# Kernel optimization log

Measured on AMD Instinct MI355X. Metric: run time of the kernel, lower is better.

## Reference

```python
import jax, jax.numpy as jnp
import numpy as np

TEMPERATURE = 0.07
NEG = -1e9  # stand-in for -inf on the diagonal; exp(NEG) == 0


def setup_inputs() -> dict:
    key = jax.random.key(0)
    k1, k2, k3 = jax.random.split(key, 3)
    B, D = 4096, 1024
    return {
        "anchor_features": jax.random.normal(k1, (B, D), dtype=jnp.float32),
        "positive_features": jax.random.normal(k2, (B, D), dtype=jnp.float32),
        "labels": jax.random.randint(k3, (B,), 0, 2),
    }


def reference(anchor_features, positive_features, labels):
    B = anchor_features.shape[0]
    # L2-normalize (normalize=True)
    a = anchor_features / jnp.linalg.norm(anchor_features, axis=1, keepdims=True)
    p = positive_features / jnp.linalg.norm(positive_features, axis=1, keepdims=True)
    feats = jnp.concatenate([a, p], axis=0)                      # [2B, D]
    sim = jnp.matmul(feats, feats.T) / TEMPERATURE               # [2B, 2B]
    diag = jnp.eye(2 * B, dtype=bool)
    sim = jnp.where(diag, NEG, sim)                              # mask self-similarity
    # logsumexp over all non-self entries per row (diag contributes exp(NEG)=0)
    lse = jax.nn.logsumexp(sim, axis=1)                          # [2B]
    # positive pair similarity: sim[i, i+B] == sim[i+B, i] == <a_i, p_i>/t
    cross = jnp.sum(a * p, axis=1) / TEMPERATURE                 # [B]
    pos_sim = jnp.concatenate([cross, cross])                    # [2B]
    lab = jnp.concatenate([labels, labels]).astype(sim.dtype)    # [2B], 0/1
    per_row = (-pos_sim + lse) * lab
    num_pos = jnp.sum(lab)
    return jnp.where(num_pos > 0, jnp.sum(per_row) / num_pos, jnp.float32(0.0))
```

## Files before the change

kernel.cpp:

```cpp
#include <hip/hip_runtime.h>
#include <hip/hip_bf16.h>

#define TEMP_INV (1.0f / 0.07f)
#define LOG2E 1.4426950408889634f
#define LN2 0.6931471805599453f
#define CFIX 21.0f

typedef __attribute__((ext_vector_type(4))) float f32x4;

__global__ __launch_bounds__(256) void norm_kernel(
    const float* __restrict__ A, const float* __restrict__ P,
    unsigned char* __restrict__ Fr, float* __restrict__ cross,
    float* __restrict__ lsum, int B, int D) {
  const int row = blockIdx.x;
  const int t = threadIdx.x;
  {
    const int zi = row * 256 + t;
    if (zi < 2 * B) lsum[zi] = 0.f;
  }
  const float4* a4 = reinterpret_cast<const float4*>(A + (size_t)row * D);
  const float4* p4 = reinterpret_cast<const float4*>(P + (size_t)row * D);
  const int n4 = D >> 2;
  float sa = 0.f, sp = 0.f, sx = 0.f;
  for (int i = t; i < n4; i += 256) {
    float4 av = a4[i], pv = p4[i];
    sa += av.x * av.x + av.y * av.y + av.z * av.z + av.w * av.w;
    sp += pv.x * pv.x + pv.y * pv.y + pv.z * pv.z + pv.w * pv.w;
    sx += av.x * pv.x + av.y * pv.y + av.z * pv.z + av.w * pv.w;
  }
#pragma unroll
  for (int off = 32; off; off >>= 1) {
    sa += __shfl_down(sa, off);
    sp += __shfl_down(sp, off);
    sx += __shfl_down(sx, off);
  }
  __shared__ float red[3][4];
  const int wid = t >> 6, lane = t & 63;
  if (lane == 0) { red[0][wid] = sa; red[1][wid] = sp; red[2][wid] = sx; }
  __syncthreads();
  sa = red[0][0] + red[0][1] + red[0][2] + red[0][3];
  sp = red[1][0] + red[1][1] + red[1][2] + red[1][3];
  sx = red[2][0] + red[2][1] + red[2][2] + red[2][3];
  const float ian = rsqrtf(sa), ipn = rsqrtf(sp);
  const float ia = ian * 16.f, ip = ipn * 16.f;
  const int NN16 = (2 * B) >> 4;
  const size_t KBSTR = (size_t)NN16 * 512;
  const int kb = t >> 3, hi = (t >> 1) & 3, half = (t & 1) * 4;
  const int rbA = row >> 4, rbP = (B + row) >> 4;
  const int lo = row & 15;
  const size_t off8 = (size_t)kb * KBSTR + ((hi << 4) + lo) * 8 + half;
  for (int i = t; i < n4; i += 256) {
    float4 av = a4[i], pv = p4[i];
    int qa = 0, qp = 0;
    qa = __builtin_amdgcn_cvt_pk_fp8_f32(av.x * ia, av.y * ia, qa, false);
    qa = __builtin_amdgcn_cvt_pk_fp8_f32(av.z * ia, av.w * ia, qa, true);
    qp = __builtin_amdgcn_cvt_pk_fp8_f32(pv.x * ip, pv.y * ip, qp, false);
    qp = __builtin_amdgcn_cvt_pk_fp8_f32(pv.z * ip, pv.w * ip, qp, true);
    *reinterpret_cast<int*>(Fr + off8 + (size_t)rbA * 512) = qa;
    *reinterpret_cast<int*>(Fr + off8 + (size_t)rbP * 512) = qp;
  }
  if (t == 0) cross[row] = sx * ian * ipn;
}

__global__ __launch_bounds__(256) void gram_kernel(
    const unsigned char* __restrict__ Fr, float* __restrict__ lsum, int NN,
    int D) {
  const int nrb = NN >> 7;
  const int ntri = nrb * (nrb + 1) / 2;
  int lin = blockIdx.x;
  lin = (lin & 7) * (ntri >> 3) + (lin >> 3);
  int by = (int)((sqrtf(8.f * (float)lin + 1.f) - 1.f) * 0.5f);
  while ((by + 1) * (by + 2) / 2 <= lin) ++by;
  while (by * (by + 1) / 2 > lin) --by;
  const int bx = lin - by * (by + 1) / 2;
  const int r0 = bx * 128;
  const int c0 = by * 128;
  const bool diag = (bx == by);

  const int t = threadIdx.x;
  const int lane = t & 63, w = t >> 6;
  const int lo = lane & 15, hi = lane >> 4;
  const int wr = w >> 1, wn = w & 1;

  const size_t KBSTR = (size_t)(NN >> 4) * 512;
  const unsigned char* pA =
      Fr + (size_t)((c0 >> 4) + wr * 4) * 512 + (size_t)lane * 8;
  const unsigned char* pB =
      Fr + (size_t)((r0 >> 4) + wn * 4) * 512 + (size_t)lane * 8;

  f32x4 acc[4][4];
#pragma unroll
  for (int a = 0; a < 4; ++a)
#pragma unroll
    for (int bb = 0; bb < 4; ++bb) acc[a][bb] = (f32x4){0.f, 0.f, 0.f, 0.f};

  long aP[4], bP[4], aQ[4], bQ[4];
#pragma unroll
  for (int q = 0; q < 4; ++q) {
    aP[q] = *(const long*)(pA + q * 512);
    bP[q] = *(const long*)(pB + q * 512);
  }

#pragma unroll 1
  for (int kb = 0; kb < 32; kb += 2) {
#pragma unroll
    for (int q = 0; q < 4; ++q) {
      aQ[q] = *(const long*)(pA + KBSTR + q * 512);
      bQ[q] = *(const long*)(pB + KBSTR + q * 512);
    }
    __builtin_amdgcn_s_setprio(1);
#pragma unroll
    for (int mf = 0; mf < 4; ++mf)
#pragma unroll
      for (int nf = 0; nf < 4; ++nf)
        acc[mf][nf] = __builtin_amdgcn_mfma_f32_16x16x32_fp8_fp8(
            aP[mf], bP[nf], acc[mf][nf], 0, 0, 0);
    __builtin_amdgcn_s_setprio(0);
    pA += 2 * KBSTR;
    pB += 2 * KBSTR;
    if (kb + 2 < 32) {
#pragma unroll
      for (int q = 0; q < 4; ++q) {
        aP[q] = *(const long*)(pA + q * 512);
        bP[q] = *(const long*)(pB + q * 512);
      }
    }
    __builtin_amdgcn_s_setprio(1);
#pragma unroll
    for (int mf = 0; mf < 4; ++mf)
#pragma unroll
      for (int nf = 0; nf < 4; ++nf)
        acc[mf][nf] = __builtin_amdgcn_mfma_f32_16x16x32_fp8_fp8(
            aQ[mf], bQ[nf], acc[mf][nf], 0, 0, 0);
    __builtin_amdgcn_s_setprio(0);
  }

  const float scl = LOG2E * TEMP_INV / 256.f;
  float s_i[4] = {0.f, 0.f, 0.f, 0.f};
  float s_j[16];
#pragma unroll
  for (int q = 0; q < 16; ++q) s_j[q] = 0.f;
  {
    const int dgb = (r0 + wn * 64) - (c0 + wr * 64);
#pragma unroll
    for (int nf = 0; nf < 4; ++nf) {
      const int dg = dgb + nf * 16 + lo;
#pragma unroll
      for (int mf = 0; mf < 4; ++mf)
#pragma unroll
        for (int rg = 0; rg < 4; ++rg) {
          const int jloc = mf * 16 + hi * 4 + rg;
          float e = exp2f(acc[mf][nf][rg] * scl - CFIX);
          if (diag && dg == jloc) e = 0.f;
          s_i[nf] += e;
          s_j[mf * 4 + rg] += e;
        }
    }
  }
#pragma unroll
  for (int nf = 0; nf < 4; ++nf) {
    float v = s_i[nf];
    v += __shfl_xor(v, 16);
    v += __shfl_xor(v, 32);
    if (hi == 0) atomicAdd(&lsum[r0 + wn * 64 + nf * 16 + lo], v);
  }
  if (!diag) {
#pragma unroll
    for (int q = 0; q < 16; ++q) {
      float v = s_j[q];
      v += __shfl_xor(v, 1);
      v += __shfl_xor(v, 2);
      v += __shfl_xor(v, 4);
      v += __shfl_xor(v, 8);
      if (lo == 0)
        atomicAdd(&lsum[c0 + wr * 64 + (q >> 2) * 16 + hi * 4 + (q & 3)], v);
    }
  }
}

__global__ __launch_bounds__(1024) void finalize_kernel(
    const float* __restrict__ lsum, const float* __restrict__ cross,
    const int* __restrict__ labels, float* __restrict__ out, int B) {
  const int NN = 2 * B;
  const int t = threadIdx.x;
  float sum = 0.f, cnt = 0.f;
  for (int i = t; i < NN; i += 1024) {
    const float lse = LN2 * (CFIX + log2f(lsum[i]));
    const float lab = (float)labels[i % B];
    sum += (lse - cross[i % B] * TEMP_INV) * lab;
    cnt += lab;
  }
#pragma unroll
  for (int off = 32; off; off >>= 1) {
    sum += __shfl_down(sum, off);
    cnt += __shfl_down(cnt, off);
  }
  __shared__ float rs[16], rc[16];
  const int wid = t >> 6, lane = t & 63;
  if (lane == 0) { rs[wid] = sum; rc[wid] = cnt; }
  __syncthreads();
  if (t == 0) {
    float S = 0.f, C = 0.f;
    for (int q = 0; q < 16; ++q) { S += rs[q]; C += rc[q]; }
    out[0] = (C > 0.f) ? S / C : 0.f;
  }
}

extern "C" void kernel_launch(void* const* d_in, const int* in_sizes, int n_in,
                              void* d_out, int out_size, void* d_ws, size_t ws_size,
                              hipStream_t stream) {
  const float* A = (const float*)d_in[0];
  const float* P = (const float*)d_in[1];
  const int* labels = (const int*)d_in[2];
  float* out = (float*)d_out;
  const int B = in_sizes[2];
  const int D = in_sizes[0] / B;
  const int NN = 2 * B;

  char* ws = (char*)d_ws;
  unsigned char* Fr = (unsigned char*)ws;
  size_t off = (size_t)NN * D;
  off = (off + 255) & ~(size_t)255;
  float* cross = (float*)(ws + off);
  off += (size_t)B * sizeof(float);
  off = (off + 255) & ~(size_t)255;
  float* lsum = (float*)(ws + off);

  norm_kernel<<<B, 256, 0, stream>>>(A, P, Fr, cross, lsum, B, D);
  const int nrb = NN >> 7;
  const int ntri = nrb * (nrb + 1) / 2;
  gram_kernel<<<ntri, 256, 0, stream>>>(Fr, lsum, NN, D);
  finalize_kernel<<<1, 1024, 0, stream>>>(lsum, cross, labels, out, B);
}
```

Measured before the change: 116.8 us.

## Stage fp8 fragments through LDS in norm kernel; deepen gram prefetch pipeline

The norm kernel now handles 16 rows per block. It quantizes them into shared memory, then writes the MFMA-fragment layout as coalesced 8-byte stores instead of scattered 4-byte stores. The gram kernel's two-stage register double buffer becomes a four-stage rotating prefetch, so global loads run further ahead of the MFMAs. The cost is about 33KB of LDS per norm block, fewer norm blocks, and higher register pressure in the gram kernel, which may lower occupancy.

New measurement: 121.6 us. 4.1% more time.

```diff
diff --git a/kernel.cpp b/kernel.cpp
--- a/kernel.cpp
+++ b/kernel.cpp
@@ -8,58 +8,75 @@
 
 typedef __attribute__((ext_vector_type(4))) float f32x4;
 
+
+#define LQS 1048
 __global__ __launch_bounds__(256) void norm_kernel(
     const float* __restrict__ A, const float* __restrict__ P,
     unsigned char* __restrict__ Fr, float* __restrict__ cross,
     float* __restrict__ lsum, int B, int D) {
-  const int row = blockIdx.x;
+  __shared__ unsigned char lq[32 * LQS];
+  __shared__ float nrm[16][2];
+  const int b = blockIdx.x;
   const int t = threadIdx.x;
   {
-    const int zi = row * 256 + t;
+    const int zi = b * 256 + t;
     if (zi < 2 * B) lsum[zi] = 0.f;
   }
-  const float4* a4 = reinterpret_cast<const float4*>(A + (size_t)row * D);
-  const float4* p4 = reinterpret_cast<const float4*>(P + (size_t)row * D);
+  const int lo16 = t >> 4, sub = t & 15;
+  const int ga = b * 16 + lo16;
+  const float4* a4 = reinterpret_cast<const float4*>(A + (size_t)ga * D);
+  const float4* p4 = reinterpret_cast<const float4*>(P + (size_t)ga * D);
   const int n4 = D >> 2;
+
   float sa = 0.f, sp = 0.f, sx = 0.f;
-  for (int i = t; i < n4; i += 256) {
+  for (int i = sub; i < n4; i += 16) {
     float4 av = a4[i], pv = p4[i];
     sa += av.x * av.x + av.y * av.y + av.z * av.z + av.w * av.w;
     sp += pv.x * pv.x + pv.y * pv.y + pv.z * pv.z + pv.w * pv.w;
     sx += av.x * pv.x + av.y * pv.y + av.z * pv.z + av.w * pv.w;
   }
 #pragma unroll
-  for (int off = 32; off; off >>= 1) {
-    sa += __shfl_down(sa, off);
-    sp += __shfl_down(sp, off);
-    sx += __shfl_down(sx, off);
-  }
-  __shared__ float red[3][4];
-  const int wid = t >> 6, lane = t & 63;
-  if (lane == 0) { red[0][wid] = sa; red[1][wid] = sp; red[2][wid] = sx; }
+  for (int off = 8; off; off >>= 1) {
+    sa += __shfl_xor(sa, off);
+    sp += __shfl_xor(sp, off);
+    sx += __shfl_xor(sx, off);
+  }
+  if (sub == 0) {
+    const float ian = rsqrtf(sa), ipn = rsqrtf(sp);
+    nrm[lo16][0] = ian;
+    nrm[lo16][1] = ipn;
+    cross[ga] = sx * ian * ipn;
+  }
   __syncthreads();
-  sa = red[0][0] + red[0][1] + red[0][2] + red[0][3];
-  sp = red[1][0] + red[1][1] + red[1][2] + red[1][3];
-  sx = red[2][0] + red[2][1] + red[2][2] + red[2][3];
-  const float ian = rsqrtf(sa), ipn = rsqrtf(sp);
-  const float ia = ian * 16.f, ip = ipn * 16.f;
-  const int NN16 = (2 * B) >> 4;
-  const size_t KBSTR = (size_t)NN16 * 512;
-  const int kb = t >> 3, hi = (t >> 1) & 3, half = (t & 1) * 4;
-  const int rbA = row >> 4, rbP = (B + row) >> 4;
-  const int lo = row & 15;
-  const size_t off8 = (size_t)kb * KBSTR + ((hi << 4) + lo) * 8 + half;
-  for (int i = t; i < n4; i += 256) {
+
+  const float ia = nrm[lo16][0] * 16.f, ip = nrm[lo16][1] * 16.f;
+  unsigned char* la = &lq[lo16 * LQS];
+  unsigned char* lp = &lq[(16 + lo16) * LQS];
+  for (int i = sub; i < n4; i += 16) {
     float4 av = a4[i], pv = p4[i];
     int qa = 0, qp = 0;
     qa = __builtin_amdgcn_cvt_pk_fp8_f32(av.x * ia, av.y * ia, qa, false);
     qa = __builtin_amdgcn_cvt_pk_fp8_f32(av.z * ia, av.w * ia, qa, true);
     qp = __builtin_amdgcn_cvt_pk_fp8_f32(pv.x * ip, pv.y * ip, qp, false);
     qp = __builtin_amdgcn_cvt_pk_fp8_f32(pv.z * ip, pv.w * ip, qp, true);
-    *reinterpret_cast<int*>(Fr + off8 + (size_t)rbA * 512) = qa;
-    *reinterpret_cast<int*>(Fr + off8 + (size_t)rbP * 512) = qp;
-  }
-  if (t == 0) cross[row] = sx * ian * ipn;
+    *reinterpret_cast<int*>(la + i * 4) = qa;
+    *reinterpret_cast<int*>(lp + i * 4) = qp;
+  }
+  __syncthreads();
+
+  const int pos = t & 63, wv = t >> 6;
+  const int flo = pos & 15, fhi = pos >> 4;
+  const size_t KBSTR = (size_t)((2 * B) >> 4) * 512;
+#pragma unroll
+  for (int s = 0; s < 16; ++s) {
+    const int f = s * 4 + wv;
+    const int rbsel = f >> 5, kb = f & 31;
+    const int rb = (rbsel == 0) ? b : ((B >> 4) + b);
+    const long v = *reinterpret_cast<const long*>(
+        &lq[(rbsel * 16 + flo) * LQS + kb * 32 + fhi * 8]);
+    *reinterpret_cast<long*>(Fr + (size_t)kb * KBSTR + (size_t)rb * 512 +
+                             pos * 8) = v;
+  }
 }
 
 __global__ __launch_bounds__(256) void gram_kernel(
@@ -94,45 +111,44 @@
 #pragma unroll
     for (int bb = 0; bb < 4; ++bb) acc[a][bb] = (f32x4){0.f, 0.f, 0.f, 0.f};
 
-  long aP[4], bP[4], aQ[4], bQ[4];
-#pragma unroll
-  for (int q = 0; q < 4; ++q) {
-    aP[q] = *(const long*)(pA + q * 512);
-    bP[q] = *(const long*)(pB + q * 512);
-  }
+#define LOADST(ar, br, KB)                                        \
+  do {                                                            \
+    const size_t o_ = (size_t)(KB)*KBSTR;                         \
+    _Pragma("unroll") for (int q = 0; q < 4; ++q) {               \
+      ar[q] = *(const long*)(pA + o_ + q * 512);                  \
+      br[q] = *(const long*)(pB + o_ + q * 512);                  \
+    }                                                             \
+  } while (0)
+
+#define MFMAS(ar, br)                                             \
+  do {                                                            \
+    __builtin_amdgcn_s_setprio(1);                                \
+    _Pragma("unroll") for (int mf = 0; mf < 4; ++mf)              \
+      _Pragma("unroll") for (int nf = 0; nf < 4; ++nf)            \
+          acc[mf][nf] = __builtin_amdgcn_mfma_f32_16x16x32_fp8_fp8( \
+              ar[mf], br[nf], acc[mf][nf], 0, 0, 0);              \
+    __builtin_amdgcn_s_setprio(0);                                \
+  } while (0)
+
+  long a0[4], b0[4], a1[4], b1[4], a2[4], b2[4], a3[4], b3[4];
+  LOADST(a0, b0, 0);
+  LOADST(a1, b1, 1);
+  LOADST(a2, b2, 2);
 
 #pragma unroll 1
-  for (int kb = 0; kb < 32; kb += 2) {
-#pragma unroll
-    for (int q = 0; q < 4; ++q) {
-      aQ[q] = *(const long*)(pA + KBSTR + q * 512);
-      bQ[q] = *(const long*)(pB + KBSTR + q * 512);
-    }
-    __builtin_amdgcn_s_setprio(1);
-#pragma unroll
-    for (int mf = 0; mf < 4; ++mf)
-#pragma unroll
-      for (int nf = 0; nf < 4; ++nf)
-        acc[mf][nf] = __builtin_amdgcn_mfma_f32_16x16x32_fp8_fp8(
-            aP[mf], bP[nf], acc[mf][nf], 0, 0, 0);
-    __builtin_amdgcn_s_setprio(0);
-    pA += 2 * KBSTR;
-    pB += 2 * KBSTR;
-    if (kb + 2 < 32) {
-#pragma unroll
-      for (int q = 0; q < 4; ++q) {
-        aP[q] = *(const long*)(pA + q * 512);
-        bP[q] = *(const long*)(pB + q * 512);
-      }
-    }
-    __builtin_amdgcn_s_setprio(1);
-#pragma unroll
-    for (int mf = 0; mf < 4; ++mf)
-#pragma unroll
-      for (int nf = 0; nf < 4; ++nf)
-        acc[mf][nf] = __builtin_amdgcn_mfma_f32_16x16x32_fp8_fp8(
-            aQ[mf], bQ[nf], acc[mf][nf], 0, 0, 0);
-    __builtin_amdgcn_s_setprio(0);
+  for (int kb = 0; kb < 32; kb += 4) {
+    const int k3 = (kb + 3 < 32) ? kb + 3 : 31;
+    const int k4 = (kb + 4 < 32) ? kb + 4 : 31;
+    const int k5 = (kb + 5 < 32) ? kb + 5 : 31;
+    const int k6 = (kb + 6 < 32) ? kb + 6 : 31;
+    LOADST(a3, b3, k3);
+    MFMAS(a0, b0);
+    LOADST(a0, b0, k4);
+    MFMAS(a1, b1);
+    LOADST(a1, b1, k5);
+    MFMAS(a2, b2);
+    LOADST(a2, b2, k6);
+    MFMAS(a3, b3);
   }
 
   const float scl = LOG2E * TEMP_INV / 256.f;
@@ -176,6 +192,8 @@
         atomicAdd(&lsum[c0 + wr * 64 + (q >> 2) * 16 + hi * 4 + (q & 3)], v);
     }
   }
+#undef LOADST
+#undef MFMAS
 }
 
 __global__ __launch_bounds__(1024) void finalize_kernel(
@@ -226,7 +244,7 @@
   off = (off + 255) & ~(size_t)255;
   float* lsum = (float*)(ws + off);
 
-  norm_kernel<<<B, 256, 0, stream>>>(A, P, Fr, cross, lsum, B, D);
+  norm_kernel<<<B / 16, 256, 0, stream>>>(A, P, Fr, cross, lsum, B, D);
   const int nrb = NN >> 7;
   const int ntri = nrb * (nrb + 1) / 2;
   gram_kernel<<<ntri, 256, 0, stream>>>(Fr, lsum, NN, D);
```
